# Kernel optimization log

Measured on AMD Instinct MI355X. Metric: run time of the kernel, lower is better.

Reference implementation:

```python
import jax, jax.numpy as jnp
import numpy as np

B, S, NQ, FFN, EMB = 8, 4096, 8, 2048, 512


def setup_inputs() -> dict:
    key = jax.random.key(0)
    k0, k1, k2, k3 = jax.random.split(key, 4)
    x = jax.random.normal(k0, (B, S, NQ), dtype=jnp.float32)
    theta = jax.random.normal(k1, (NQ,), dtype=jnp.float32)  # trainable RY angles
    W1 = jax.random.normal(k2, (NQ, FFN), dtype=jnp.float32) / np.float32(np.sqrt(NQ))
    b1 = jnp.zeros((FFN,), dtype=jnp.float32)
    W2 = jax.random.normal(k3, (FFN, EMB), dtype=jnp.float32) / np.float32(np.sqrt(FFN))
    b2 = jnp.zeros((EMB,), dtype=jnp.float32)
    return {"x": x, "theta": theta, "W1": W1, "b1": b1, "W2": W2, "b2": b2}


def reference(x, theta, W1, b1, W2, b2):
    # Quantum layer: per wire i, state RY(theta_i) RX(x_i) |0>; no entangling gates,
    # so the state is a product state and <PauliZ_i> = cos(x_i) * cos(theta_i) exactly.
    # This fuses the per-token / per-gate simulation loop into one batched expression.
    q = jnp.cos(x) * jnp.cos(theta)                     # [B, S, NQ]
    # Dropout is identity at eval time.
    h = jax.nn.relu(jnp.einsum("bsq,qf->bsf", q, W1) + b1)  # [B, S, FFN]
    out = jnp.einsum("bsf,fe->bse", h, W2) + b2             # [B, S, EMB]
    return out
```

## Files before the change

### kernel.cpp

```cpp
#include <hip/hip_runtime.h>

#define T_TOK 32768
#define NQ    8
#define FFN   2048
#define EMB   512
#define BM    128
#define BN    256
#define BK    32
#define NCHUNK (FFN / BK)

typedef __attribute__((ext_vector_type(8)))  short short8;
typedef __attribute__((ext_vector_type(16))) float f32x16;
typedef __attribute__((ext_vector_type(2)))  unsigned int u32x2;

__device__ __forceinline__ unsigned short f2bf(float f) {
  unsigned int u = __float_as_uint(f);
  u += 0x7fffu + ((u >> 16) & 1u);
  return (unsigned short)(u >> 16);
}

__device__ __forceinline__ unsigned pk2bf(float lo, float hi) {
#if __has_builtin(__builtin_amdgcn_cvt_pk_bf16_f32)
  typedef __attribute__((ext_vector_type(2))) __bf16 bf2;
  bf2 p = __builtin_amdgcn_cvt_pk_bf16_f32(lo, hi);
  return *(unsigned*)&p;
#else
  return (unsigned)f2bf(lo) | ((unsigned)f2bf(hi) << 16);
#endif
}

__global__ void prep_all(const float* __restrict__ W1,
                         const float* __restrict__ b1,
                         const float* __restrict__ W2,
                         unsigned short* __restrict__ w1t,
                         unsigned short* __restrict__ w2t) {
  __shared__ float t[32][33];
  const int kb = blockIdx.x * 32;
  const int nb = blockIdx.y * 32;
  const int tid = threadIdx.x;
  const int c = tid & 31, r0 = tid >> 5;
#pragma unroll
  for (int p = 0; p < 4; ++p) {
    int r = r0 + p * 8;
    t[r][c] = W2[(size_t)(kb + r) * EMB + nb + c];
  }
  __syncthreads();
#pragma unroll
  for (int p = 0; p < 4; ++p) {
    int r = r0 + p * 8;
    w2t[(size_t)(nb + r) * FFN + kb + c] = f2bf(t[c][r]);
  }
  if (blockIdx.x == 0) {
    const int f     = blockIdx.y * 128 + (tid >> 1);
    const int khalf = tid & 1;
    unsigned short v8[8];
#pragma unroll
    for (int j = 0; j < 8; ++j) {
      const int k = khalf * 8 + j;
      float val = (k < 8) ? W1[(size_t)k * FFN + f]
                          : (k == 8 ? b1[f] : 0.f);
      v8[j] = f2bf(val);
    }
    *(uint4*)(w1t + (size_t)f * 16 + khalf * 8) = *(uint4*)v8;
  }
}

__global__ __launch_bounds__(256, 2) void ffq_main(
    const float* __restrict__ x,
    const float* __restrict__ theta,
    const unsigned short* __restrict__ w1t,
    const unsigned short* __restrict__ w2t,
    const float* __restrict__ b2,
    float* __restrict__ out) {

  __shared__ __align__(16) unsigned short w2_lds[2][BN * BK];

  const int tid  = threadIdx.x;
  const int wave = tid >> 6;
  const int lane = tid & 63;
  const int nl   = lane & 31;
  const int hi   = lane >> 5;
  const int tok0 = blockIdx.x * BM;
  const int n0   = blockIdx.y * BN;

  float cth[8];
  {
    const float4* tp = (const float4*)theta;
    float4 t0 = tp[0], t1 = tp[1];
    cth[0] = __cosf(t0.x); cth[1] = __cosf(t0.y);
    cth[2] = __cosf(t0.z); cth[3] = __cosf(t0.w);
    cth[4] = __cosf(t1.x); cth[5] = __cosf(t1.y);
    cth[6] = __cosf(t1.z); cth[7] = __cosf(t1.w);
  }
  short8 bq;
  {
    const float4* xp =
        (const float4*)(x + (size_t)(tok0 + wave * 32 + nl) * NQ);
    float4 x0 = xp[0], x1 = xp[1];
    float q0 = __cosf(x0.x) * cth[0], q1 = __cosf(x0.y) * cth[1];
    float q2 = __cosf(x0.z) * cth[2], q3 = __cosf(x0.w) * cth[3];
    float q4 = __cosf(x1.x) * cth[4], q5 = __cosf(x1.y) * cth[5];
    float q6 = __cosf(x1.z) * cth[6], q7 = __cosf(x1.w) * cth[7];
    uint4 uu;
    uu.x = pk2bf(q0, q1); uu.y = pk2bf(q2, q3);
    uu.z = pk2bf(q4, q5); uu.w = pk2bf(q6, q7);
    if (hi) { uu.x = 0x00003f80u; uu.y = 0; uu.z = 0; uu.w = 0; }
    bq = *(short8*)&uu;
  }

  const int st_gc = (tid & 3) ^ ((tid >> 3) & 3);
  auto stage_w2 = [&](int kc_, int b_) {
    const int k0_ = kc_ * BK;
#pragma unroll
    for (int issue = 0; issue < 4; ++issue) {
      const int r = issue * 64 + (tid >> 2);
      __builtin_amdgcn_global_load_lds(
          (const __attribute__((address_space(1))) void*)(
              w2t + (size_t)(n0 + r) * FFN + k0_ + st_gc * 8),
          (__attribute__((address_space(3))) void*)(
              &w2_lds[b_][issue * 2048 + tid * 8]),
          16, 0, 0);
    }
  };

  const int swz  = (nl >> 1) & 3;
  const int off0 = nl * 32 + ((0 + hi) ^ swz) * 8;
  const int off1 = nl * 32 + ((2 + hi) ^ swz) * 8;

  f32x16 acc[8];
#pragma unroll
  for (int nt = 0; nt < 8; ++nt)
#pragma unroll
    for (int r = 0; r < 16; ++r) acc[nt][r] = 0.f;

  auto gemm1 = [&](short8 aw, short8& oA, short8& oB) {
    f32x16 c1;
#pragma unroll
    for (int r = 0; r < 16; ++r) c1[r] = 0.f;
    c1 = __builtin_amdgcn_mfma_f32_32x32x16_bf16(aw, bq, c1, 0, 0, 0);
    unsigned Q[8];
#pragma unroll
    for (int p = 0; p < 8; ++p) {
      float lo = c1[2 * p]     > 0.f ? c1[2 * p]     : 0.f;
      float hl = c1[2 * p + 1] > 0.f ? c1[2 * p + 1] : 0.f;
      Q[p] = pk2bf(lo, hl);
    }
    u32x2 s0 = __builtin_amdgcn_permlane32_swap(Q[0], Q[2], false, false);
    u32x2 s1 = __builtin_amdgcn_permlane32_swap(Q[1], Q[3], false, false);
    u32x2 s2 = __builtin_amdgcn_permlane32_swap(Q[4], Q[6], false, false);
    u32x2 s3 = __builtin_amdgcn_permlane32_swap(Q[5], Q[7], false, false);
    uint4 uA; uA.x = s0[0]; uA.y = s1[0]; uA.z = s0[1]; uA.w = s1[1];
    uint4 uB; uB.x = s2[0]; uB.y = s3[0]; uB.z = s2[1]; uB.w = s3[1];
    oA = *(short8*)&uA;
    oB = *(short8*)&uB;
  };

  short8 afA_c, afB_c, afA_n, afB_n;
  {
    stage_w2(0, 0);
    short8 aw0 = *(const short8*)(w1t + (size_t)nl * 16 + hi * 8);
    gemm1(aw0, afA_c, afB_c);
  }

#pragma unroll 2
  for (int kc = 0; kc < NCHUNK; ++kc) {
    const int b  = kc & 1;
    const int nc = (kc + 1 < NCHUNK) ? kc + 1 : NCHUNK - 1;

    asm volatile("s_waitcnt vmcnt(0)" ::: "memory");
    __builtin_amdgcn_s_barrier();
    __builtin_amdgcn_sched_barrier(0);

    short8 aw = *(const short8*)(w1t + (size_t)(nc * BK + nl) * 16 + hi * 8);

    stage_w2(nc, b ^ 1);

    const unsigned short* sb = &w2_lds[b][0];
#pragma unroll
    for (int nt = 0; nt < 8; ++nt) {
      short8 bf = *(const short8*)(sb + off0 + nt * 1024);
      acc[nt] = __builtin_amdgcn_mfma_f32_32x32x16_bf16(
          afA_c, bf, acc[nt], 0, 0, 0);
    }
#pragma unroll
    for (int nt = 0; nt < 8; ++nt) {
      short8 bf = *(const short8*)(sb + off1 + nt * 1024);
      acc[nt] = __builtin_amdgcn_mfma_f32_32x32x16_bf16(
          afB_c, bf, acc[nt], 0, 0, 0);
    }

    gemm1(aw, afA_n, afB_n);
    afA_c = afA_n;
    afB_c = afB_n;
  }

  asm volatile("s_waitcnt vmcnt(0)" ::: "memory");

#pragma unroll
  for (int nt = 0; nt < 8; ++nt) {
    const int col = n0 + nt * 32 + nl;
    const float bv = b2[col];
    const int rbase = tok0 + wave * 32 + 4 * hi;
#pragma unroll
    for (int g2 = 0; g2 < 4; ++g2)
#pragma unroll
      for (int rr = 0; rr < 4; ++rr)
        out[(size_t)(rbase + 8 * g2 + rr) * EMB + col] =
            acc[nt][4 * g2 + rr] + bv;
  }
}

extern "C" void kernel_launch(void* const* d_in, const int* in_sizes, int n_in,
                              void* d_out, int out_size, void* d_ws, size_t ws_size,
                              hipStream_t stream) {
  const float* x     = (const float*)d_in[0];
  const float* theta = (const float*)d_in[1];
  const float* W1    = (const float*)d_in[2];
  const float* b1    = (const float*)d_in[3];
  const float* W2    = (const float*)d_in[4];
  const float* b2    = (const float*)d_in[5];
  float* out = (float*)d_out;

  unsigned short* w1t = (unsigned short*)d_ws;
  unsigned short* w2t = w1t + FFN * 16;

  prep_all<<<dim3(FFN / 32, EMB / 32), 256, 0, stream>>>(W1, b1, W2, w1t, w2t);

  dim3 grid(T_TOK / BM, EMB / BN);
  ffq_main<<<grid, 256, 0, stream>>>(x, theta, w1t, w2t, b2, out);
}
```

Before: 158.0 us.

## Reshape block tile to 256 tokens by 128 outputs with two token groups per wave

Changes the block tile from 128x256 to 256x128. Each wave now computes two 32-token groups, so every W2 fragment read from LDS feeds two MFMAs, and each block stages half as much W2 per chunk. The cost is that the first GEMM, with its ReLU, bf16 packing and permlane swaps, runs twice per wave per chunk. It is also recomputed across four column blocks instead of two, which doubles that hidden-activation work overall.

```diff
diff --git a/kernel.cpp b/kernel.cpp
--- a/kernel.cpp
+++ b/kernel.cpp
@@ -4,8 +4,8 @@
 #define NQ    8
 #define FFN   2048
 #define EMB   512
-#define BM    128
-#define BN    256
+#define BM    256
+#define BN    128
 #define BK    32
 #define NCHUNK (FFN / BK)
 
@@ -92,10 +92,11 @@
     cth[4] = __cosf(t1.x); cth[5] = __cosf(t1.y);
     cth[6] = __cosf(t1.z); cth[7] = __cosf(t1.w);
   }
-  short8 bq;
-  {
-    const float4* xp =
-        (const float4*)(x + (size_t)(tok0 + wave * 32 + nl) * NQ);
+  short8 bq0, bq1;
+#pragma unroll
+  for (int g = 0; g < 2; ++g) {
+    const float4* xp = (const float4*)(
+        x + (size_t)(tok0 + wave * 64 + g * 32 + nl) * NQ);
     float4 x0 = xp[0], x1 = xp[1];
     float q0 = __cosf(x0.x) * cth[0], q1 = __cosf(x0.y) * cth[1];
     float q2 = __cosf(x0.z) * cth[2], q3 = __cosf(x0.w) * cth[3];
@@ -105,14 +106,14 @@
     uu.x = pk2bf(q0, q1); uu.y = pk2bf(q2, q3);
     uu.z = pk2bf(q4, q5); uu.w = pk2bf(q6, q7);
     if (hi) { uu.x = 0x00003f80u; uu.y = 0; uu.z = 0; uu.w = 0; }
-    bq = *(short8*)&uu;
+    if (g == 0) bq0 = *(short8*)&uu; else bq1 = *(short8*)&uu;
   }
 
   const int st_gc = (tid & 3) ^ ((tid >> 3) & 3);
   auto stage_w2 = [&](int kc_, int b_) {
     const int k0_ = kc_ * BK;
 #pragma unroll
-    for (int issue = 0; issue < 4; ++issue) {
+    for (int issue = 0; issue < 2; ++issue) {
       const int r = issue * 64 + (tid >> 2);
       __builtin_amdgcn_global_load_lds(
           (const __attribute__((address_space(1))) void*)(
@@ -129,11 +130,11 @@
 
   f32x16 acc[8];
 #pragma unroll
-  for (int nt = 0; nt < 8; ++nt)
-#pragma unroll
-    for (int r = 0; r < 16; ++r) acc[nt][r] = 0.f;
-
-  auto gemm1 = [&](short8 aw, short8& oA, short8& oB) {
+  for (int i = 0; i < 8; ++i)
+#pragma unroll
+    for (int r = 0; r < 16; ++r) acc[i][r] = 0.f;
+
+  auto gemm1 = [&](short8 aw, short8 bq, short8& oA, short8& oB) {
     f32x16 c1;
 #pragma unroll
     for (int r = 0; r < 16; ++r) c1[r] = 0.f;
@@ -155,12 +156,16 @@
     oB = *(short8*)&uB;
   };
 
-  short8 afA_c, afB_c, afA_n, afB_n;
+  short8 afA0_c, afB0_c, afA1_c, afB1_c;
+  short8 afA0_n, afB0_n, afA1_n, afB1_n;
   {
     stage_w2(0, 0);
     short8 aw0 = *(const short8*)(w1t + (size_t)nl * 16 + hi * 8);
-    gemm1(aw0, afA_c, afB_c);
-  }
+    gemm1(aw0, bq0, afA0_c, afB0_c);
+    gemm1(aw0, bq1, afA1_c, afB1_c);
+  }
+
+#define MF(a, b, c) __builtin_amdgcn_mfma_f32_32x32x16_bf16((a), (b), (c), 0, 0, 0)
 
 #pragma unroll 2
   for (int kc = 0; kc < NCHUNK; ++kc) {
@@ -176,37 +181,43 @@
     stage_w2(nc, b ^ 1);
 
     const unsigned short* sb = &w2_lds[b][0];
-#pragma unroll
-    for (int nt = 0; nt < 8; ++nt) {
+
+#pragma unroll
+    for (int nt = 0; nt < 4; ++nt) {
       short8 bf = *(const short8*)(sb + off0 + nt * 1024);
-      acc[nt] = __builtin_amdgcn_mfma_f32_32x32x16_bf16(
-          afA_c, bf, acc[nt], 0, 0, 0);
-    }
-#pragma unroll
-    for (int nt = 0; nt < 8; ++nt) {
+      acc[nt]     = MF(afA0_c, bf, acc[nt]);
+      acc[4 + nt] = MF(afA1_c, bf, acc[4 + nt]);
+    }
+#pragma unroll
+    for (int nt = 0; nt < 4; ++nt) {
       short8 bf = *(const short8*)(sb + off1 + nt * 1024);
-      acc[nt] = __builtin_amdgcn_mfma_f32_32x32x16_bf16(
-          afB_c, bf, acc[nt], 0, 0, 0);
-    }
-
-    gemm1(aw, afA_n, afB_n);
-    afA_c = afA_n;
-    afB_c = afB_n;
-  }
+      acc[nt]     = MF(afB0_c, bf, acc[nt]);
+      acc[4 + nt] = MF(afB1_c, bf, acc[4 + nt]);
+    }
+
+    gemm1(aw, bq0, afA0_n, afB0_n);
+    gemm1(aw, bq1, afA1_n, afB1_n);
+    afA0_c = afA0_n; afB0_c = afB0_n;
+    afA1_c = afA1_n; afB1_c = afB1_n;
+  }
+#undef MF
 
   asm volatile("s_waitcnt vmcnt(0)" ::: "memory");
 
 #pragma unroll
-  for (int nt = 0; nt < 8; ++nt) {
-    const int col = n0 + nt * 32 + nl;
-    const float bv = b2[col];
-    const int rbase = tok0 + wave * 32 + 4 * hi;
-#pragma unroll
-    for (int g2 = 0; g2 < 4; ++g2)
-#pragma unroll
-      for (int rr = 0; rr < 4; ++rr)
-        out[(size_t)(rbase + 8 * g2 + rr) * EMB + col] =
-            acc[nt][4 * g2 + rr] + bv;
+  for (int g = 0; g < 2; ++g) {
+#pragma unroll
+    for (int nt = 0; nt < 4; ++nt) {
+      const int col = n0 + nt * 32 + nl;
+      const float bv = b2[col];
+      const int rbase = tok0 + wave * 64 + g * 32 + 4 * hi;
+#pragma unroll
+      for (int g2 = 0; g2 < 4; ++g2)
+#pragma unroll
+        for (int rr = 0; rr < 4; ++rr)
+          out[(size_t)(rbase + 8 * g2 + rr) * EMB + col] =
+              acc[g * 4 + nt][4 * g2 + rr] + bv;
+    }
   }
 }
 
```

New measurement: 163.6 us. 1.04x slower.
